# Performance work log

Hardware: AMD Instinct MI355X
Metric: run time of the kernel (lower is better)

## Reference

```python
import jax, jax.numpy as jnp
import numpy as np

N = 50000
E = 800000
D_IN = 128
D_HID = 128
NUM_LAYERS = 3


def setup_inputs() -> dict:
    key = jax.random.key(0)
    ks = jax.random.split(key, 8)
    x = jax.random.normal(ks[0], (N, D_IN), dtype=jnp.float32)
    edge_index = jax.random.randint(ks[1], (2, E), 0, N, dtype=jnp.int64)
    edge_weight = jnp.ones((E,), dtype=jnp.float32)
    # GCNConv params: glorot-ish weights [in, out], zero bias
    def w(k, fi, fo):
        return jax.random.normal(k, (fi, fo), dtype=jnp.float32) * (1.0 / np.sqrt(fi))
    W0 = w(ks[2], D_IN, D_HID)
    b0 = jnp.zeros((D_HID,), dtype=jnp.float32)
    W1 = w(ks[3], D_HID, D_HID)
    b1 = jnp.zeros((D_HID,), dtype=jnp.float32)
    W2 = w(ks[4], D_HID, D_HID)
    b2 = jnp.zeros((D_HID,), dtype=jnp.float32)
    return {"x": x, "edge_index": edge_index, "edge_weight": edge_weight,
            "W0": W0, "b0": b0, "W1": W1, "b1": b1, "W2": W2, "b2": b2}


def _gcn_layer(h, src, dst, norm, W, b, n):
    # linear transform then degree-normalized scatter-add aggregation
    h = h @ W                                   # [N, d_out]
    msg = h[src] * norm[:, None]                # gather + scale, [E+N, d_out]
    out = jax.ops.segment_sum(msg, dst, num_segments=n)  # scatter-add
    return out + b


def reference(x, edge_index, edge_weight, W0, b0, W1, b1, W2, b2):
    n = x.shape[0]
    loop = jnp.arange(n, dtype=edge_index.dtype)
    src = jnp.concatenate([edge_index[0], loop])   # add self-loops (fill=1)
    dst = jnp.concatenate([edge_index[1], loop])
    ew = jnp.concatenate([edge_weight, jnp.ones((n,), dtype=edge_weight.dtype)])
    # symmetric normalization: deg computed on target (col), norm = d^-1/2[src]*w*d^-1/2[dst]
    deg = jax.ops.segment_sum(ew, dst, num_segments=n)
    dis = jnp.where(deg > 0, jax.lax.rsqrt(deg), 0.0)
    norm = dis[src] * ew * dis[dst]               # [E+N]
    z = x
    for (W, b) in ((W0, b0), (W1, b1), (W2, b2)):
        z = _gcn_layer(z, src, dst, norm, W, b, n)
        z = jax.nn.relu(z)
    return z
```

## Files before the change

kernel.cpp:

```cpp
#include <hip/hip_runtime.h>

#define D 128
#define NB 250
#define BN 200
#define NBLK 128
#define CAP 7168

typedef float f2v __attribute__((ext_vector_type(2)));
typedef short bf16x8 __attribute__((ext_vector_type(8)));
typedef float f32x4 __attribute__((ext_vector_type(4)));

__device__ __forceinline__ unsigned bf16r(float f) {
  unsigned u = __float_as_uint(f);
  return (u + 0x7fffu + ((u >> 16) & 1u)) >> 16;
}


__global__ __launch_bounds__(256) void k_pre1(const int* __restrict__ dst, int* __restrict__ M, int E,
                                              const float* __restrict__ X, unsigned short* __restrict__ Xb,
                                              int total4, int GC,
                                              const float* __restrict__ W0, const float* __restrict__ W1,
                                              const float* __restrict__ W2, unsigned short* __restrict__ Wt) {
  __shared__ int lh[NB];
  int b = blockIdx.x;
  int tid = threadIdx.x;
  if (b < NBLK) {
    for (int i = tid; i < NB; i += 256) lh[i] = 0;
    __syncthreads();
    const int EPB = (E + NBLK - 1) / NBLK;
    int e0 = b * EPB;
    int e1 = min(e0 + EPB, E);
    for (int e = e0 + tid; e < e1; e += 256) atomicAdd(&lh[dst[e] / BN], 1);
    __syncthreads();
    for (int i = tid; i < NB; i += 256) M[b * NB + i] = lh[i];
  } else if (b < NBLK + GC) {
    int i = (b - NBLK) * 256 + tid;
    if (i < total4) {
      float4 v = ((const float4*)X)[i];
      ushort4 o;
      o.x = (unsigned short)bf16r(v.x);
      o.y = (unsigned short)bf16r(v.y);
      o.z = (unsigned short)bf16r(v.z);
      o.w = (unsigned short)bf16r(v.w);
      ((ushort4*)Xb)[i] = o;
    }
  } else {
    int i = (b - NBLK - GC) * 256 + tid;
    if (i < 3 * 16384) {
      int l = i >> 14;
      int r = i & 16383;
      int nn = r >> 7, kk = r & 127;
      const float* W = (l == 0) ? W0 : (l == 1) ? W1 : W2;
      Wt[i] = (unsigned short)bf16r(W[kk * 128 + nn]);
    }
  }
}


__global__ __launch_bounds__(256) void k_mscan(int* __restrict__ M, int* __restrict__ bbase, int Etot) {
  __shared__ int s[256];
  int t = threadIdx.x;
  int v = 0;
  if (t < NB) {
    for (int blk = 0; blk < NBLK; ++blk) v += M[blk * NB + t];
  }
  s[t] = v;
  __syncthreads();
#pragma unroll
  for (int off = 1; off < 256; off <<= 1) {
    int u = (t >= off) ? s[t - off] : 0;
    __syncthreads();
    s[t] += u;
    __syncthreads();
  }
  int ex = s[t] - v;
  if (t < NB) {
    bbase[t] = ex;
    int run = ex;
    for (int blk = 0; blk < NBLK; ++blk) {
      int c = M[blk * NB + t];
      M[blk * NB + t] = run;
      run += c;
    }
  }
  if (t == 0) bbase[NB] = Etot;
}


__global__ __launch_bounds__(256) void k_pre2(const unsigned short* __restrict__ Zb,
                                              const unsigned short* __restrict__ Wt,
                                              unsigned short* __restrict__ H, int n, int GG,
                                              const int* __restrict__ src, const int* __restrict__ dst,
                                              const float* __restrict__ ew, const int* __restrict__ M,
                                              uint2* __restrict__ part, int E) {
  __shared__ int lcur[NB];
  int b = blockIdx.x;
  if (b < GG) {
    int lane = threadIdx.x & 63;
    int wid  = threadIdx.x >> 6;
    int row0 = b * 16;
    int r  = lane & 15;
    int kg = lane >> 4;
    int c0 = wid * 32;
    const size_t abase  = (size_t)(row0 + r) * 128 + kg * 8;
    const size_t b0base = (size_t)(c0 + r) * 128 + kg * 8;
    const size_t b1base = (size_t)(c0 + 16 + r) * 128 + kg * 8;
    f32x4 acc0 = {0.f, 0.f, 0.f, 0.f};
    f32x4 acc1 = {0.f, 0.f, 0.f, 0.f};
#pragma unroll
    for (int k0 = 0; k0 < 128; k0 += 32) {
      bf16x8 a  = *(const bf16x8*)&Zb[abase + k0];
      bf16x8 b0 = *(const bf16x8*)&Wt[b0base + k0];
      bf16x8 b1 = *(const bf16x8*)&Wt[b1base + k0];
      acc0 = __builtin_amdgcn_mfma_f32_16x16x32_bf16(a, b0, acc0, 0, 0, 0);
      acc1 = __builtin_amdgcn_mfma_f32_16x16x32_bf16(a, b1, acc1, 0, 0, 0);
    }
    int orow = row0 + kg * 4;
#pragma unroll
    for (int j = 0; j < 4; ++j) {
      H[(size_t)(orow + j) * 128 + c0 + r]      = (unsigned short)bf16r(acc0[j]);
      H[(size_t)(orow + j) * 128 + c0 + 16 + r] = (unsigned short)bf16r(acc1[j]);
    }
  } else {
    int blk = b - GG;
    int tid = threadIdx.x;
    for (int i = tid; i < NB; i += 256) lcur[i] = M[blk * NB + i];
    __syncthreads();
    const int EPB = (E + NBLK - 1) / NBLK;
    int e0 = blk * EPB;
    int e1 = min(e0 + EPB, E);
    for (int e = e0 + tid; e < e1; e += 256) {
      int d = dst[e];
      int bkt = d / BN;
      int dlow = d - bkt * BN;
      int p = atomicAdd(&lcur[bkt], 1);
      uint2 rec;
      rec.x = (unsigned)src[e] | ((unsigned)dlow << 24);
      rec.y = __float_as_uint(ew[e]);
      part[p] = rec;
    }
  }
}


__global__ __launch_bounds__(256) void k_bsort(const uint2* __restrict__ part, const int* __restrict__ bbase,
                                               uint2* __restrict__ csr, int* __restrict__ rowptr,
                                               float* __restrict__ dis, int n, int E) {
  __shared__ uint2 stage[CAP];
  __shared__ int lh[BN];
  __shared__ float ldeg[BN];
  __shared__ int s[256];
  int b = blockIdx.x;
  int tid = threadIdx.x;
  int base = bbase[b];
  int cnt = bbase[b + 1] - base;
  for (int i = tid; i < BN; i += 256) { lh[i] = 0; ldeg[i] = 0.f; }
  __syncthreads();
  for (int i = tid; i < cnt; i += 256) {
    uint2 r = part[base + i];
    if (i < CAP) stage[i] = r;
    int dlow = r.x >> 24;
    atomicAdd(&lh[dlow], 1);
    atomicAdd(&ldeg[dlow], __uint_as_float(r.y));
  }
  __syncthreads();
  int v = (tid < BN) ? lh[tid] : 0;
  s[tid] = v;
  __syncthreads();
#pragma unroll
  for (int off = 1; off < 256; off <<= 1) {
    int u = (tid >= off) ? s[tid - off] : 0;
    __syncthreads();
    s[tid] += u;
    __syncthreads();
  }
  int ex = s[tid] - v;
  if (tid < BN) {
    lh[tid] = ex;
    int node = b * BN + tid;
    rowptr[node] = base + ex;
    dis[node] = rsqrtf(1.0f + ldeg[tid]);
  }
  if (b == 0 && tid == 0) rowptr[n] = E;
  __syncthreads();
  for (int i = tid; i < cnt; i += 256) {
    uint2 r = (i < CAP) ? stage[i] : part[base + i];
    int dlow = r.x >> 24;
    int p = atomicAdd(&lh[dlow], 1);
    uint2 o;
    o.x = r.x & 0x00FFFFFFu;
    o.y = r.y;
    csr[base + p] = o;
  }
}


__global__ __launch_bounds__(256) void k_gemm(const unsigned short* __restrict__ Zb,
                                              const unsigned short* __restrict__ Wt,
                                              unsigned short* __restrict__ H, int n) {
  int lane = threadIdx.x & 63;
  int wid  = threadIdx.x >> 6;
  int row0 = blockIdx.x * 16;
  int r  = lane & 15;
  int kg = lane >> 4;
  int c0 = wid * 32;
  const size_t abase  = (size_t)(row0 + r) * 128 + kg * 8;
  const size_t b0base = (size_t)(c0 + r) * 128 + kg * 8;
  const size_t b1base = (size_t)(c0 + 16 + r) * 128 + kg * 8;
  f32x4 acc0 = {0.f, 0.f, 0.f, 0.f};
  f32x4 acc1 = {0.f, 0.f, 0.f, 0.f};
#pragma unroll
  for (int k0 = 0; k0 < 128; k0 += 32) {
    bf16x8 a  = *(const bf16x8*)&Zb[abase + k0];
    bf16x8 b0 = *(const bf16x8*)&Wt[b0base + k0];
    bf16x8 b1 = *(const bf16x8*)&Wt[b1base + k0];
    acc0 = __builtin_amdgcn_mfma_f32_16x16x32_bf16(a, b0, acc0, 0, 0, 0);
    acc1 = __builtin_amdgcn_mfma_f32_16x16x32_bf16(a, b1, acc1, 0, 0, 0);
  }
  int orow = row0 + kg * 4;
#pragma unroll
  for (int j = 0; j < 4; ++j) {
    H[(size_t)(orow + j) * 128 + c0 + r]      = (unsigned short)bf16r(acc0[j]);
    H[(size_t)(orow + j) * 128 + c0 + 16 + r] = (unsigned short)bf16r(acc1[j]);
  }
}


__global__ __launch_bounds__(256) void k_agg(const unsigned* __restrict__ Hb, const int* __restrict__ rowptr,
                                             const f2v* __restrict__ csr, const float* __restrict__ dis,
                                             const float* __restrict__ bias, unsigned* __restrict__ outb,
                                             float* __restrict__ outf, int n) {
  int node = __builtin_amdgcn_readfirstlane(blockIdx.x * 4 + (threadIdx.x >> 6));
  if (node >= n) return;
  int lane = threadIdx.x & 63;
  float ax = 0.f, ay = 0.f;
  int e = rowptr[node];
  const int end = rowptr[node + 1];
  for (; e + 4 <= end; e += 4) {
    f2v r0 = __builtin_nontemporal_load(&csr[e]);
    f2v r1 = __builtin_nontemporal_load(&csr[e + 1]);
    f2v r2 = __builtin_nontemporal_load(&csr[e + 2]);
    f2v r3 = __builtin_nontemporal_load(&csr[e + 3]);
    int s0 = __float_as_int(r0.x);
    int s1 = __float_as_int(r1.x);
    int s2 = __float_as_int(r2.x);
    int s3 = __float_as_int(r3.x);
    float w0 = r0.y * dis[s0];
    float w1 = r1.y * dis[s1];
    float w2 = r2.y * dis[s2];
    float w3 = r3.y * dis[s3];
    unsigned g0 = Hb[(size_t)s0 * 64 + lane];
    unsigned g1 = Hb[(size_t)s1 * 64 + lane];
    unsigned g2 = Hb[(size_t)s2 * 64 + lane];
    unsigned g3 = Hb[(size_t)s3 * 64 + lane];
    ax = fmaf(__uint_as_float(g0 << 16), w0, ax); ay = fmaf(__uint_as_float(g0 & 0xffff0000u), w0, ay);
    ax = fmaf(__uint_as_float(g1 << 16), w1, ax); ay = fmaf(__uint_as_float(g1 & 0xffff0000u), w1, ay);
    ax = fmaf(__uint_as_float(g2 << 16), w2, ax); ay = fmaf(__uint_as_float(g2 & 0xffff0000u), w2, ay);
    ax = fmaf(__uint_as_float(g3 << 16), w3, ax); ay = fmaf(__uint_as_float(g3 & 0xffff0000u), w3, ay);
  }
  for (; e < end; ++e) {
    f2v r0 = __builtin_nontemporal_load(&csr[e]);
    int s0 = __float_as_int(r0.x);
    float w0 = r0.y * dis[s0];
    unsigned g0 = Hb[(size_t)s0 * 64 + lane];
    ax = fmaf(__uint_as_float(g0 << 16), w0, ax); ay = fmaf(__uint_as_float(g0 & 0xffff0000u), w0, ay);
  }
  float dn = dis[node];
  float sn = dn * dn;
  unsigned hv = Hb[(size_t)node * 64 + lane];
  float hvx = __uint_as_float(hv << 16);
  float hvy = __uint_as_float(hv & 0xffff0000u);
  float2 bv = ((const float2*)bias)[lane];
  float ox = fmaxf(fmaf(dn, ax, fmaf(sn, hvx, bv.x)), 0.f);
  float oy = fmaxf(fmaf(dn, ay, fmaf(sn, hvy, bv.y)), 0.f);
  if (outb) {
    outb[(size_t)node * 64 + lane] = bf16r(ox) | (bf16r(oy) << 16);
  } else {
    f2v o; o.x = ox; o.y = oy;
    __builtin_nontemporal_store(o, (f2v*)outf + (size_t)node * 64 + lane);
  }
}


extern "C" void kernel_launch(void* const* d_in, const int* in_sizes, int n_in,
                              void* d_out, int out_size, void* d_ws, size_t ws_size,
                              hipStream_t stream) {
  const float* x  = (const float*)d_in[0];
  const int*   ei = (const int*)d_in[1];
  const float* ew = (const float*)d_in[2];
  const float* W0 = (const float*)d_in[3];
  const float* W1 = (const float*)d_in[5];
  const float* W2 = (const float*)d_in[7];
  const float* bl[3] = {(const float*)d_in[4], (const float*)d_in[6], (const float*)d_in[8]};

  const int n = in_sizes[0] / D;
  const int E = in_sizes[1] / 2;
  const int* src = ei;
  const int* dst = ei + E;

  char* p = (char*)d_ws;
  unsigned short* Zb     = (unsigned short*)p; p += (size_t)n * D * 2;
  unsigned short* H      = (unsigned short*)p; p += (size_t)n * D * 2;
  float*          dis    = (float*)p;          p += (size_t)n * 4;
  int*            rowptr = (int*)p;            p += (size_t)(n + 1) * 4;
  int*            M      = (int*)p;            p += (size_t)NBLK * NB * 4;
  int*            bbase  = (int*)p;            p += (size_t)(NB + 1) * 4;
  uint2*          part   = (uint2*)p;          p += (size_t)E * 8;
  uint2*          csr    = (uint2*)p;          p += (size_t)E * 8;
  unsigned short* Wt     = (unsigned short*)p; p += 3 * 16384 * 2;
  (void)ws_size; (void)n_in;

  const int total4 = n * D / 4;
  const int GC = (total4 + 255) / 256;
  const int GW = (3 * 16384 + 255) / 256;
  const int GG = n / 16;

  k_pre1<<<NBLK + GC + GW, 256, 0, stream>>>(dst, M, E, x, Zb, total4, GC, W0, W1, W2, Wt);
  k_mscan<<<1, 256, 0, stream>>>(M, bbase, E);
  k_pre2<<<GG + NBLK, 256, 0, stream>>>(Zb, Wt, H, n, GG, src, dst, ew, M, part, E);
  k_bsort<<<NB, 256, 0, stream>>>(part, bbase, csr, rowptr, dis, n, E);

  float* outp = (float*)d_out;
  k_agg<<<(n + 3) / 4, 256, 0, stream>>>((const unsigned*)H, rowptr, (const f2v*)csr, dis, bl[0], (unsigned*)Zb, outp, n);
  for (int l = 1; l < 3; ++l) {
    k_gemm<<<GG, 256, 0, stream>>>(Zb, Wt + l * 16384, H, n);
    unsigned* ob = (l == 2) ? nullptr : (unsigned*)Zb;
    k_agg<<<(n + 3) / 4, 256, 0, stream>>>((const unsigned*)H, rowptr, (const f2v*)csr, dis, bl[l], ob, outp, n);
  }
}
```

Measured before the change: 224.3 us.

## Quadruple histogram blocks and replace serial bucket scan with three-pass parallel scan

Raises the number of edge-partitioning blocks from 128 to 512 so the histogram and scatter phases have more parallelism. The count matrix is transposed to bucket-major order, so that one flat exclusive scan produces both per-block offsets and bucket bases. The single-block serial scan is replaced by three kernels: block sums, a scan of those sums, and a local scan. This adds two kernel launches and a larger count matrix in exchange for removing a latency-bound serial loop and underused scatter blocks.

```diff
diff --git a/kernel.cpp b/kernel.cpp
--- a/kernel.cpp
+++ b/kernel.cpp
@@ -3,7 +3,7 @@
 #define D 128
 #define NB 250
 #define BN 200
-#define NBLK 128
+#define NBLK 512
 #define CAP 7168
 
 typedef float f2v __attribute__((ext_vector_type(2)));
@@ -32,7 +32,7 @@
     int e1 = min(e0 + EPB, E);
     for (int e = e0 + tid; e < e1; e += 256) atomicAdd(&lh[dst[e] / BN], 1);
     __syncthreads();
-    for (int i = tid; i < NB; i += 256) M[b * NB + i] = lh[i];
+    for (int i = tid; i < NB; i += 256) M[i * NBLK + b] = lh[i];
   } else if (b < NBLK + GC) {
     int i = (b - NBLK) * 256 + tid;
     if (i < total4) {
@@ -57,13 +57,39 @@
 }
 
 
-__global__ __launch_bounds__(256) void k_mscan(int* __restrict__ M, int* __restrict__ bbase, int Etot) {
+__global__ __launch_bounds__(256) void k_blocksum(const int* __restrict__ cnt, int* __restrict__ bsum, int n) {
+  int i = blockIdx.x * 256 + threadIdx.x;
+  int v = (i < n) ? cnt[i] : 0;
+#pragma unroll
+  for (int off = 32; off > 0; off >>= 1) v += __shfl_down(v, off);
+  __shared__ int ws[4];
+  if ((threadIdx.x & 63) == 0) ws[threadIdx.x >> 6] = v;
+  __syncthreads();
+  if (threadIdx.x == 0) bsum[blockIdx.x] = ws[0] + ws[1] + ws[2] + ws[3];
+}
+
+__global__ __launch_bounds__(512) void k_scanb2(const int* __restrict__ bsum, int* __restrict__ boff, int nb) {
+  __shared__ int s[512];
+  int t = threadIdx.x;
+  int v = (t < nb) ? bsum[t] : 0;
+  s[t] = v;
+  __syncthreads();
+#pragma unroll
+  for (int off = 1; off < 512; off <<= 1) {
+    int u = (t >= off) ? s[t - off] : 0;
+    __syncthreads();
+    s[t] += u;
+    __syncthreads();
+  }
+  if (t < nb) boff[t] = s[t] - v;
+}
+
+__global__ __launch_bounds__(256) void k_scanm(int* __restrict__ M, const int* __restrict__ boff,
+                                               int* __restrict__ bbase, int flatN, int Etot) {
   __shared__ int s[256];
   int t = threadIdx.x;
-  int v = 0;
-  if (t < NB) {
-    for (int blk = 0; blk < NBLK; ++blk) v += M[blk * NB + t];
-  }
+  int i = blockIdx.x * 256 + t;
+  int v = (i < flatN) ? M[i] : 0;
   s[t] = v;
   __syncthreads();
 #pragma unroll
@@ -73,17 +99,12 @@
     s[t] += u;
     __syncthreads();
   }
-  int ex = s[t] - v;
-  if (t < NB) {
-    bbase[t] = ex;
-    int run = ex;
-    for (int blk = 0; blk < NBLK; ++blk) {
-      int c = M[blk * NB + t];
-      M[blk * NB + t] = run;
-      run += c;
-    }
-  }
-  if (t == 0) bbase[NB] = Etot;
+  int ex = s[t] - v + boff[blockIdx.x];
+  if (i < flatN) {
+    M[i] = ex;
+    if ((i & (NBLK - 1)) == 0) bbase[i / NBLK] = ex;
+  }
+  if (i == 0) bbase[NB] = Etot;
 }
 
 
@@ -124,7 +145,7 @@
   } else {
     int blk = b - GG;
     int tid = threadIdx.x;
-    for (int i = tid; i < NB; i += 256) lcur[i] = M[blk * NB + i];
+    for (int i = tid; i < NB; i += 256) lcur[i] = M[i * NBLK + blk];
     __syncthreads();
     const int EPB = (E + NBLK - 1) / NBLK;
     int e0 = blk * EPB;
@@ -303,8 +324,10 @@
   unsigned short* H      = (unsigned short*)p; p += (size_t)n * D * 2;
   float*          dis    = (float*)p;          p += (size_t)n * 4;
   int*            rowptr = (int*)p;            p += (size_t)(n + 1) * 4;
-  int*            M      = (int*)p;            p += (size_t)NBLK * NB * 4;
+  int*            M      = (int*)p;            p += (size_t)NB * NBLK * 4;
   int*            bbase  = (int*)p;            p += (size_t)(NB + 1) * 4;
+  int*            bsum2  = (int*)p;            p += 512 * 4;
+  int*            boff2  = (int*)p;            p += 512 * 4;
   uint2*          part   = (uint2*)p;          p += (size_t)E * 8;
   uint2*          csr    = (uint2*)p;          p += (size_t)E * 8;
   unsigned short* Wt     = (unsigned short*)p; p += 3 * 16384 * 2;
@@ -314,9 +337,13 @@
   const int GC = (total4 + 255) / 256;
   const int GW = (3 * 16384 + 255) / 256;
   const int GG = n / 16;
+  const int flatN = NB * NBLK;
+  const int GS = flatN / 256;
 
   k_pre1<<<NBLK + GC + GW, 256, 0, stream>>>(dst, M, E, x, Zb, total4, GC, W0, W1, W2, Wt);
-  k_mscan<<<1, 256, 0, stream>>>(M, bbase, E);
+  k_blocksum<<<GS, 256, 0, stream>>>(M, bsum2, flatN);
+  k_scanb2<<<1, 512, 0, stream>>>(bsum2, boff2, GS);
+  k_scanm<<<GS, 256, 0, stream>>>(M, boff2, bbase, flatN, E);
   k_pre2<<<GG + NBLK, 256, 0, stream>>>(Zb, Wt, H, n, GG, src, dst, ew, M, part, E);
   k_bsort<<<NB, 256, 0, stream>>>(part, bbase, csr, rowptr, dis, n, E);
 
```

Measured after the change: 213.9 us. -4.6%, faster.
